# Performance work log

Hardware: AMD Instinct MI355X
Metric: run time of the kernel (lower is better)

## Reference

```python
import jax, jax.numpy as jnp
import numpy as np

B, N, D, H = 8, 1024, 512, 8
DH = D // H  # 64
ALPHA = 0.2  # LeakyReLU slope (args.alpha)
EPS = 1e-6
NEG = -1e9


def layer_norm(x, g, b):
    mean = jnp.mean(x, axis=-1, keepdims=True)
    std = jnp.std(x, axis=-1, keepdims=True)
    return g * (x - mean) / (std + EPS) + b


def setup_inputs() -> dict:
    key = jax.random.key(0)
    ks = jax.random.split(key, 6)
    x = jax.random.normal(ks[0], (B, N, D), dtype=jnp.float32)
    mask = jnp.zeros((B, N), dtype=jnp.int32)  # unused by the block body
    adj = jax.random.randint(ks[1], (B, N, N), 0, 2).astype(jnp.int32)
    W = jax.random.normal(ks[2], (H, D, DH), dtype=jnp.float32) * 0.05
    a_src = jax.random.normal(ks[3], (H, DH), dtype=jnp.float32) * 0.05
    a_dst = jax.random.normal(ks[4], (H, DH), dtype=jnp.float32) * 0.05
    ln1_g = jnp.ones((D,), jnp.float32)
    ln1_b = jnp.zeros((D,), jnp.float32)
    ln2_g = jnp.ones((D,), jnp.float32)
    ln2_b = jnp.zeros((D,), jnp.float32)
    return {"x": x, "mask": mask, "adj": adj, "W": W, "a_src": a_src,
            "a_dst": a_dst, "ln1_g": ln1_g, "ln1_b": ln1_b,
            "ln2_g": ln2_g, "ln2_b": ln2_b}


def ggat(xn, adj, W, a_src, a_dst):
    # multi-head GAT-style attention over dense adjacency (inputP)
    h = jnp.einsum('bnd,hdk->bhnk', xn, W)                 # [B,H,N,DH]
    f_src = jnp.einsum('bhnk,hk->bhn', h, a_src)           # [B,H,N]
    f_dst = jnp.einsum('bhnk,hk->bhn', h, a_dst)
    e = jax.nn.leaky_relu(f_src[..., :, None] + f_dst[..., None, :], ALPHA)
    e = jnp.where(adj[:, None, :, :] > 0, e, NEG)          # mask non-edges
    attn = jax.nn.softmax(e, axis=-1)                      # [B,H,N,N]
    out = jnp.einsum('bhnm,bhmk->bhnk', attn, h)           # aggregate
    out = out.transpose(0, 2, 1, 3).reshape(out.shape[0], out.shape[2], -1)
    return jax.nn.elu(out)                                 # [B,N,D]


def reference(x, mask, adj, W, a_src, a_dst, ln1_g, ln1_b, ln2_g, ln2_b):
    # SublayerConnection: x + dropout(sublayer(norm(x))); dropout = identity (eval)
    xn = layer_norm(x, ln1_g, ln1_b)
    y = x + ggat(xn, adj, W, a_src, a_dst)
    # extra LayerNorm + dropout(identity); module returns (dropout(x), 0)
    y = layer_norm(y, ln2_g, ln2_b)
    return y
```

## Files before the change

### kernel.cpp

```cpp
#include <hip/hip_runtime.h>
#include <stdint.h>

#define B_ 8
#define N_ 1024
#define D_ 512
#define H_ 8
#define DH_ 64


using bf16x8 = __attribute__((ext_vector_type(8))) __bf16;
using f32x4  = __attribute__((ext_vector_type(4))) float;

__device__ __forceinline__ float bf2f(uint32_t u) {
  union { uint32_t u; float f; } c; c.u = u << 16; return c.f;
}
__device__ __forceinline__ uint16_t f2bf(float f) {
  union { float f; uint32_t u; } c; c.f = f;
  return (uint16_t)((c.u + 0x7FFFu + ((c.u >> 16) & 1u)) >> 16);
}
__device__ __forceinline__ void load8f(const void* p, size_t idx, int f32, float v[8]) {
  if (f32) {
    const float4* q = (const float4*)((const float*)p + idx);
    float4 a = q[0], b = q[1];
    v[0]=a.x; v[1]=a.y; v[2]=a.z; v[3]=a.w; v[4]=b.x; v[5]=b.y; v[6]=b.z; v[7]=b.w;
  } else {
    uint4 u = *(const uint4*)((const uint16_t*)p + idx);
    const uint32_t* w = (const uint32_t*)&u;
#pragma unroll
    for (int e = 0; e < 4; e++) { v[2*e] = bf2f(w[e] & 0xffffu); v[2*e+1] = bf2f(w[e] >> 16); }
  }
}
__device__ __forceinline__ float load1f(const void* p, size_t idx, int f32) {
  return f32 ? ((const float*)p)[idx] : bf2f(((const uint16_t*)p)[idx]);
}

__device__ __forceinline__ int detect_f32_block(const uint16_t* x, int t, int* sflag) {
  if (t == 0) *sflag = 0;
  __syncthreads();
  uint2 u = ((const uint2*)x)[t];
  uint32_t bad = 0;
  bad |= (((u.x >> 7)  & 0xffu) >= 0x90u);
  bad |= (((u.x >> 23) & 0xffu) >= 0x90u);
  bad |= (((u.y >> 7)  & 0xffu) >= 0x90u);
  bad |= (((u.y >> 23) & 0xffu) >= 0x90u);
  if (__any(bad)) { if ((t & 63) == 0) atomicOr(sflag, 1); }
  __syncthreads();
  return *sflag;
}

__global__ __launch_bounds__(256) void k_pp(const int* __restrict__ adj,
                                            unsigned long long* __restrict__ adjp,
                                            const uint16_t* __restrict__ xr,
                                            int* __restrict__ flag,
                                            const void* __restrict__ x,
                                            const void* __restrict__ g,
                                            const void* __restrict__ bb,
                                            uint16_t* __restrict__ xn,
                                            const void* __restrict__ W,
                                            uint16_t* __restrict__ Wt) {
  const int bx = blockIdx.x, t = threadIdx.x;
  if (bx < 2048) {
    const int row  = bx * 4 + (t >> 6);
    const int lane = t & 63;
    const int* ar = adj + (size_t)row * N_;
#pragma unroll
    for (int c = 0; c < 16; c++) {
      unsigned long long m = __ballot(ar[c * 64 + lane] > 0);
      if (lane == 0) adjp[(size_t)row * 16 + c] = m;
    }
    return;
  }
  __shared__ int sflag;
  if (bx == 2048) {
    int f32 = detect_f32_block(xr, t, &sflag);
    if (t == 0) *flag = f32;
    return;
  }
  if (bx >= 4097) {
    const int f32 = detect_f32_block(xr, t, &sflag);
    const int bw = bx - 4097;
    const int h = bw >> 3, dt = bw & 7;
    __shared__ uint16_t tile[64][65];
    const size_t sbase = ((size_t)h * D_ + dt * 64) * DH_;
    for (int e = t; e < 4096; e += 256) tile[e >> 6][e & 63] = f2bf(load1f(W, sbase + e, f32));
    __syncthreads();
    uint16_t* dst = Wt + (size_t)h * DH_ * D_ + dt * 64;
    for (int e = t; e < 4096; e += 256) {
      const int k = e >> 6, dd = e & 63;
      dst[(size_t)k * D_ + dd] = tile[dd][k];
    }
    return;
  }
  const int f32 = detect_f32_block(xr, t, &sflag);
  const int row  = (bx - 2049) * 4 + (t >> 6);
  const int lane = t & 63;
  const size_t base = (size_t)row * D_ + lane * 8;
  float v[8]; load8f(x, base, f32, v);
  float s = 0.f, sq = 0.f;
#pragma unroll
  for (int e = 0; e < 8; e++) { s += v[e]; sq += v[e] * v[e]; }
#pragma unroll
  for (int d = 32; d; d >>= 1) { s += __shfl_xor(s, d); sq += __shfl_xor(sq, d); }
  const float mean = s * (1.0f / D_);
  float var = fmaxf(sq * (1.0f / D_) - mean * mean, 0.0f);
  const float inv = 1.0f / (sqrtf(var) + 1e-6f);
  float gv[8], bv[8];
  load8f(g, lane * 8, f32, gv); load8f(bb, lane * 8, f32, bv);
  uint4 ov; uint32_t* ow = (uint32_t*)&ov;
#pragma unroll
  for (int e = 0; e < 4; e++) {
    float o0 = gv[2*e]   * ((v[2*e]   - mean) * inv) + bv[2*e];
    float o1 = gv[2*e+1] * ((v[2*e+1] - mean) * inv) + bv[2*e+1];
    ow[e] = (uint32_t)f2bf(o0) | ((uint32_t)f2bf(o1) << 16);
  }
  *(uint4*)(xn + base) = ov;
}

__global__ __launch_bounds__(256, 2) void k_gemm(const uint16_t* __restrict__ xn,
                                              const uint16_t* __restrict__ Wt,
                                              uint16_t* __restrict__ ht,
                                              const void* __restrict__ asr,
                                              const void* __restrict__ adst,
                                              float* __restrict__ fs,
                                              float* __restrict__ fd,
                                              const int* __restrict__ flag) {
  const int h = blockIdx.x;
  const int r0 = blockIdx.y * 64;
  const int t = threadIdx.x;
  const int wv = t >> 6, lane = t & 63, q = lane >> 4, m16 = lane & 15;
  const int wr = wv >> 1, wc = wv & 1;

  __shared__ union {
    struct { __align__(16) uint16_t A[64 * 72]; __align__(16) uint16_t Bt[64 * 72]; } st;
    __align__(16) uint16_t tr[64 * 72];
  } L;

  f32x4 acc[2][2] = {};
  const int srow = t >> 2, soff = (t & 3) * 16;
  const uint16_t* gA = xn + (size_t)(r0 + srow) * D_ + soff;
  const uint16_t* gB = Wt + ((size_t)h * DH_ + srow) * D_ + soff;
  uint16_t* lA = &L.st.A[srow * 72 + soff];
  uint16_t* lB = &L.st.Bt[srow * 72 + soff];

  for (int k0 = 0; k0 < D_; k0 += 64) {
    uint4 va0 = *(const uint4*)(gA + k0);
    uint4 va1 = *(const uint4*)(gA + k0 + 8);
    uint4 vb0 = *(const uint4*)(gB + k0);
    uint4 vb1 = *(const uint4*)(gB + k0 + 8);
    __syncthreads();
    *(uint4*)lA = va0;  *(uint4*)(lA + 8) = va1;
    *(uint4*)lB = vb0;  *(uint4*)(lB + 8) = vb1;
    __syncthreads();
#pragma unroll
    for (int ks = 0; ks < 2; ks++) {
      bf16x8 a0 = *(const bf16x8*)&L.st.A[(wr * 32 + m16) * 72 + ks * 32 + q * 8];
      bf16x8 a1 = *(const bf16x8*)&L.st.A[(wr * 32 + 16 + m16) * 72 + ks * 32 + q * 8];
      bf16x8 b0 = *(const bf16x8*)&L.st.Bt[(wc * 32 + m16) * 72 + ks * 32 + q * 8];
      bf16x8 b1 = *(const bf16x8*)&L.st.Bt[(wc * 32 + 16 + m16) * 72 + ks * 32 + q * 8];
      acc[0][0] = __builtin_amdgcn_mfma_f32_16x16x32_bf16(a0, b0, acc[0][0], 0, 0, 0);
      acc[0][1] = __builtin_amdgcn_mfma_f32_16x16x32_bf16(a0, b1, acc[0][1], 0, 0, 0);
      acc[1][0] = __builtin_amdgcn_mfma_f32_16x16x32_bf16(a1, b0, acc[1][0], 0, 0, 0);
      acc[1][1] = __builtin_amdgcn_mfma_f32_16x16x32_bf16(a1, b1, acc[1][1], 0, 0, 0);
    }
  }
  __syncthreads();
#pragma unroll
  for (int i2 = 0; i2 < 2; i2++)
#pragma unroll
    for (int j2 = 0; j2 < 2; j2++) {
      f32x4 vv = acc[i2][j2];
      const int sl = wr * 32 + i2 * 16 + q * 4;
      const int kl = wc * 32 + j2 * 16 + m16;
#pragma unroll
      for (int r = 0; r < 4; r++) L.tr[kl * 72 + sl + r] = f2bf(vv[r]);
    }
  __syncthreads();
  const int b = r0 >> 10, n0 = r0 & 1023;
  {
    const int k = t >> 2, ns = (t & 3) * 16;
    const size_t base = (((size_t)b * H_ + h) * DH_ + k) * (size_t)N_ + n0 + ns;
    *(uint4*)(ht + base) = *(const uint4*)&L.tr[k * 72 + ns];
    *(uint4*)(ht + base + 8) = *(const uint4*)&L.tr[k * 72 + ns + 8];
  }
  {
    const int f32 = *flag;
    const int nl = t >> 2, qd = (t & 3) * 16;
    float ss = 0.f, sd = 0.f;
#pragma unroll
    for (int dd = 0; dd < 16; dd++) {
      float hv = bf2f(L.tr[(qd + dd) * 72 + nl]);
      ss = fmaf(hv, load1f(asr,  h * DH_ + qd + dd, f32), ss);
      sd = fmaf(hv, load1f(adst, h * DH_ + qd + dd, f32), sd);
    }
    ss += __shfl_xor(ss, 1); ss += __shfl_xor(ss, 2);
    sd += __shfl_xor(sd, 1); sd += __shfl_xor(sd, 2);
    if ((t & 3) == 0) {
      fs[((size_t)b * H_ + h) * N_ + n0 + nl] = ss;
      fd[((size_t)b * H_ + h) * N_ + n0 + nl] = sd;
    }
  }
}

__global__ __launch_bounds__(256, 2) void k_attn(const uint16_t* __restrict__ ht,
                                                 const float* __restrict__ fs,
                                                 const float* __restrict__ fd,
                                                 const uint32_t* __restrict__ adjp,
                                                 uint16_t* __restrict__ oat) {
  const int bid = blockIdx.x;
  const int bh = bid & 63, itile = bid >> 6;
  const int b = bh >> 3, h = bh & 7;
  const int i0 = itile * 128;
  const int t = threadIdx.x, wv = t >> 6, lane = t & 63, q = lane >> 4, m16 = lane & 15;
  __shared__ __align__(16) uint16_t Hs[64 * 136];
  __shared__ __align__(16) float2 Edi[N_];
  for (int j = t; j < N_; j += 256) {
    float fdv = fd[(size_t)bh * N_ + j];
    Edi[j] = make_float2(exp2f(fdv * 1.44269504f), exp2f(fdv * 0.28853901f));
  }
  const int iA0 = i0 + wv * 32 + m16;
  const int iA1 = iA0 + 16;
  const float fs0 = fs[(size_t)bh * N_ + iA0];
  const float fs1 = fs[(size_t)bh * N_ + iA1];
  const float Es0  = exp2f(fs0 * 1.44269504f), Es20 = exp2f(fs0 * 0.28853901f);
  const float Es1  = exp2f(fs1 * 1.44269504f), Es21 = exp2f(fs1 * 0.28853901f);
  const uint32_t* arow0 = adjp + ((size_t)b * N_ + iA0) * 32;
  const uint32_t* arow1 = adjp + ((size_t)b * N_ + iA1) * 32;
  const uint16_t* gH = ht + (size_t)bh * (DH_ * N_) + (size_t)(t >> 2) * N_ + (t & 3) * 32;
  uint16_t* lH = &Hs[(t >> 2) * 136 + (t & 3) * 32];
  union { uint16_t u[8]; bf16x8 v; } ones;
#pragma unroll
  for (int e = 0; e < 8; e++) ones.u[e] = 0x3F80u;
  f32x4 acc[2][5] = {};
  __syncthreads();
  for (int c = 0; c < 8; c++) {
    const int jc = c * 128;
    uint4 v0 = *(const uint4*)(gH + jc);
    uint4 v1 = *(const uint4*)(gH + jc + 8);
    uint4 v2 = *(const uint4*)(gH + jc + 16);
    uint4 v3 = *(const uint4*)(gH + jc + 24);
    uint4 aw0 = *(const uint4*)(arow0 + c * 4);
    uint4 aw1 = *(const uint4*)(arow1 + c * 4);
    __syncthreads();
    *(uint4*)(lH)      = v0;
    *(uint4*)(lH + 8)  = v1;
    *(uint4*)(lH + 16) = v2;
    *(uint4*)(lH + 24) = v3;
    __syncthreads();
    const uint32_t w0[4] = {aw0.x, aw0.y, aw0.z, aw0.w};
    const uint32_t w1[4] = {aw1.x, aw1.y, aw1.z, aw1.w};
#pragma unroll
    for (int s = 0; s < 4; s++) {
      const int js = s * 32;
      bf16x8 bf0 = *(const bf16x8*)&Hs[(m16)      * 136 + js + q * 8];
      bf16x8 bf1 = *(const bf16x8*)&Hs[(16 + m16) * 136 + js + q * 8];
      bf16x8 bf2 = *(const bf16x8*)&Hs[(32 + m16) * 136 + js + q * 8];
      bf16x8 bf3 = *(const bf16x8*)&Hs[(48 + m16) * 136 + js + q * 8];
      const float2* ed = &Edi[jc + js + q * 8];
      float4 e0 = *(const float4*)(ed);
      float4 e1 = *(const float4*)(ed + 2);
      float4 e2 = *(const float4*)(ed + 4);
      float4 e3 = *(const float4*)(ed + 6);
      const uint32_t ab0 = (w0[s] >> (q * 8)) & 0xffu;
      const uint32_t ab1 = (w1[s] >> (q * 8)) & 0xffu;
#pragma unroll
      for (int f = 0; f < 2; f++) {
        const float Ea  = f ? Es1 : Es0;
        const float Eb  = f ? Es21 : Es20;
        const uint32_t ab = f ? ab1 : ab0;
        float pm[8];
        pm[0] = fmaxf(Ea * e0.x, Eb * e0.y);
        pm[1] = fmaxf(Ea * e0.z, Eb * e0.w);
        pm[2] = fmaxf(Ea * e1.x, Eb * e1.y);
        pm[3] = fmaxf(Ea * e1.z, Eb * e1.w);
        pm[4] = fmaxf(Ea * e2.x, Eb * e2.y);
        pm[5] = fmaxf(Ea * e2.z, Eb * e2.w);
        pm[6] = fmaxf(Ea * e3.x, Eb * e3.y);
        pm[7] = fmaxf(Ea * e3.z, Eb * e3.w);
        union { __bf16 bv[8]; bf16x8 v; } af;
#pragma unroll
        for (int e = 0; e < 8; e++) {
          uint32_t msk = (uint32_t)(((int32_t)(ab << (31 - e))) >> 31);
          af.bv[e] = (__bf16)__uint_as_float(__float_as_uint(pm[e]) & msk);
        }
        acc[f][0] = __builtin_amdgcn_mfma_f32_16x16x32_bf16(af.v, bf0, acc[f][0], 0, 0, 0);
        acc[f][1] = __builtin_amdgcn_mfma_f32_16x16x32_bf16(af.v, bf1, acc[f][1], 0, 0, 0);
        acc[f][2] = __builtin_amdgcn_mfma_f32_16x16x32_bf16(af.v, bf2, acc[f][2], 0, 0, 0);
        acc[f][3] = __builtin_amdgcn_mfma_f32_16x16x32_bf16(af.v, bf3, acc[f][3], 0, 0, 0);
        acc[f][4] = __builtin_amdgcn_mfma_f32_16x16x32_bf16(af.v, ones.v, acc[f][4], 0, 0, 0);
      }
    }
  }
#pragma unroll
  for (int f = 0; f < 2; f++) {
    float linv[4];
#pragma unroll
    for (int r = 0; r < 4; r++) linv[r] = 1.0f / acc[f][4][r];
    const int ibl = i0 + wv * 32 + f * 16 + q * 4;
#pragma unroll
    for (int nt = 0; nt < 4; nt++)
#pragma unroll
      for (int r = 0; r < 4; r++) {
        oat[((size_t)b * N_ + ibl + r) * D_ + h * DH_ + nt * 16 + m16] =
            f2bf(acc[f][nt][r] * linv[r]);
      }
  }
}

__global__ __launch_bounds__(256) void k_final(const void* __restrict__ x,
                                               const uint16_t* __restrict__ oa,
                                               const void* __restrict__ g,
                                               const void* __restrict__ bb,
                                               void* __restrict__ out,
                                               const int* __restrict__ flag) {
  const int f32 = *flag;
  const int row = blockIdx.x * 4 + (threadIdx.x >> 6);
  const int lane = threadIdx.x & 63;
  const size_t base = (size_t)row * D_ + lane * 8;
  float xv[8]; load8f(x, base, f32, xv);
  uint4 av = *(const uint4*)(oa + base);
  const uint32_t* aw = (const uint32_t*)&av;
  float v[8], s = 0.f, sq = 0.f;
#pragma unroll
  for (int e = 0; e < 4; e++) {
    float a0 = bf2f(aw[e] & 0xffffu), a1 = bf2f(aw[e] >> 16);
    a0 = a0 > 0.f ? a0 : exp2f(a0 * 1.44269504f) - 1.0f;
    a1 = a1 > 0.f ? a1 : exp2f(a1 * 1.44269504f) - 1.0f;
    float t0 = xv[2*e] + a0, t1 = xv[2*e+1] + a1;
    v[2*e] = t0; v[2*e+1] = t1;
    s += t0 + t1; sq += t0 * t0 + t1 * t1;
  }
#pragma unroll
  for (int d = 32; d; d >>= 1) { s += __shfl_xor(s, d); sq += __shfl_xor(sq, d); }
  const float mean = s * (1.0f / D_);
  float var = fmaxf(sq * (1.0f / D_) - mean * mean, 0.0f);
  const float inv = 1.0f / (sqrtf(var) + 1e-6f);
  float gv[8], bv[8];
  load8f(g, lane * 8, f32, gv); load8f(bb, lane * 8, f32, bv);
  float r8[8];
#pragma unroll
  for (int e = 0; e < 8; e++) r8[e] = gv[e] * ((v[e] - mean) * inv) + bv[e];
  if (f32) {
    float* o = (float*)out + base;
    float4 o0 = {r8[0], r8[1], r8[2], r8[3]};
    float4 o1 = {r8[4], r8[5], r8[6], r8[7]};
    *(float4*)(o) = o0;
    *(float4*)(o + 4) = o1;
  } else {
    uint4 ov; uint32_t* ow = (uint32_t*)&ov;
#pragma unroll
    for (int e = 0; e < 4; e++)
      ow[e] = (uint32_t)f2bf(r8[2*e]) | ((uint32_t)f2bf(r8[2*e+1]) << 16);
    *(uint4*)((uint16_t*)out + base) = ov;
  }
}

extern "C" void kernel_launch(void* const* d_in, const int* in_sizes, int n_in,
                              void* d_out, int out_size, void* d_ws, size_t ws_size,
                              hipStream_t stream) {
  const void* x = d_in[0];
  const int* adj = (const int*)d_in[2];
  const void* W = d_in[3];
  const void* asr = d_in[4];
  const void* adst = d_in[5];
  const void* g1 = d_in[6];
  const void* b1 = d_in[7];
  const void* g2 = d_in[8];
  const void* b2 = d_in[9];

  uint8_t* ws = (uint8_t*)d_ws;
  uint16_t* ht = (uint16_t*)(ws);
  uint16_t* xn = (uint16_t*)(ws + 8388608);
  uint16_t* oat = xn;
  uint16_t* Wt = (uint16_t*)(ws + 16777216);
  uint32_t* adjp = (uint32_t*)(ws + 17301504);
  float* fs = (float*)(ws + 18350080);
  float* fd = (float*)(ws + 18612224);
  int* flag = (int*)(ws + 18874368);

  k_pp<<<dim3(4161), dim3(256), 0, stream>>>(adj, (unsigned long long*)adjp,
                                             (const uint16_t*)x, flag,
                                             x, g1, b1, xn, W, Wt);
  k_gemm<<<dim3(8, 128), dim3(256), 0, stream>>>(xn, Wt, ht, asr, adst, fs, fd, flag);
  k_attn<<<dim3(512), dim3(256), 0, stream>>>(ht, fs, fd, adjp, oat);
  k_final<<<dim3(2048), dim3(256), 0, stream>>>(x, oat, g2, b2, d_out, flag);
}
```

Measured before the change: 166.7 us.

## Switch intermediates to fp16 with packed-half softmax math and register prefetch

Changes the xn, Wt, ht and attention-output intermediates from bf16 to fp16 and uses f16 MFMA. In the attention kernel the exp-weight products, max and mask are computed with packed half2 ops on fp16 LDS tables instead of per-element fp32 math and bf16 conversion. Both the GEMM and attention loops now prefetch the next tile's global loads into registers before the MMA work on the current tile. fp16 has a narrower range than bf16, so the unnormalised exp products risk overflow or underflow if the scores grow.

```diff
diff --git a/kernel.cpp b/kernel.cpp
--- a/kernel.cpp
+++ b/kernel.cpp
@@ -8,8 +8,9 @@
 #define DH_ 64
 
 
-using bf16x8 = __attribute__((ext_vector_type(8))) __bf16;
-using f32x4  = __attribute__((ext_vector_type(4))) float;
+using f16x8 = __attribute__((ext_vector_type(8))) _Float16;
+using h2    = __attribute__((ext_vector_type(2))) _Float16;
+using f32x4 = __attribute__((ext_vector_type(4))) float;
 
 __device__ __forceinline__ float bf2f(uint32_t u) {
   union { uint32_t u; float f; } c; c.u = u << 16; return c.f;
@@ -17,6 +18,35 @@
 __device__ __forceinline__ uint16_t f2bf(float f) {
   union { float f; uint32_t u; } c; c.f = f;
   return (uint16_t)((c.u + 0x7FFFu + ((c.u >> 16) & 1u)) >> 16);
+}
+__device__ __forceinline__ uint16_t f2h(float f) {
+  union { _Float16 h; uint16_t u; } c; c.h = (_Float16)f; return c.u;
+}
+__device__ __forceinline__ float h2f(uint16_t u) {
+  union { uint16_t u; _Float16 h; } c; c.u = u; return (float)c.h;
+}
+__device__ __forceinline__ uint32_t pk2h(float a, float b) {
+  union { h2 h; uint32_t u; } c; c.h = (h2){(_Float16)a, (_Float16)b}; return c.u;
+}
+__device__ __forceinline__ h2 u2h2(uint32_t u) {
+  union { uint32_t u; h2 h; } c; c.u = u; return c.h;
+}
+__device__ __forceinline__ uint32_t h22u(h2 h) {
+  union { h2 h; uint32_t u; } c; c.h = h; return c.u;
+}
+__device__ __forceinline__ h2 h2splat(float v) {
+  return (h2){(_Float16)v, (_Float16)v};
+}
+__device__ __forceinline__ h2 hmax2(h2 a, h2 b) {
+#if defined(__has_builtin)
+#if __has_builtin(__builtin_elementwise_max)
+  return __builtin_elementwise_max(a, b);
+#else
+  h2 r; r.x = a.x > b.x ? a.x : b.x; r.y = a.y > b.y ? a.y : b.y; return r;
+#endif
+#else
+  h2 r; r.x = a.x > b.x ? a.x : b.x; r.y = a.y > b.y ? a.y : b.y; return r;
+#endif
 }
 __device__ __forceinline__ void load8f(const void* p, size_t idx, int f32, float v[8]) {
   if (f32) {
@@ -82,7 +112,7 @@
     const int h = bw >> 3, dt = bw & 7;
     __shared__ uint16_t tile[64][65];
     const size_t sbase = ((size_t)h * D_ + dt * 64) * DH_;
-    for (int e = t; e < 4096; e += 256) tile[e >> 6][e & 63] = f2bf(load1f(W, sbase + e, f32));
+    for (int e = t; e < 4096; e += 256) tile[e >> 6][e & 63] = f2h(load1f(W, sbase + e, f32));
     __syncthreads();
     uint16_t* dst = Wt + (size_t)h * DH_ * D_ + dt * 64;
     for (int e = t; e < 4096; e += 256) {
@@ -111,7 +141,7 @@
   for (int e = 0; e < 4; e++) {
     float o0 = gv[2*e]   * ((v[2*e]   - mean) * inv) + bv[2*e];
     float o1 = gv[2*e+1] * ((v[2*e+1] - mean) * inv) + bv[2*e+1];
-    ow[e] = (uint32_t)f2bf(o0) | ((uint32_t)f2bf(o1) << 16);
+    ow[e] = (uint32_t)f2h(o0) | ((uint32_t)f2h(o1) << 16);
   }
   *(uint4*)(xn + base) = ov;
 }
@@ -142,25 +172,31 @@
   uint16_t* lA = &L.st.A[srow * 72 + soff];
   uint16_t* lB = &L.st.Bt[srow * 72 + soff];
 
+  uint4 va0 = *(const uint4*)(gA);
+  uint4 va1 = *(const uint4*)(gA + 8);
+  uint4 vb0 = *(const uint4*)(gB);
+  uint4 vb1 = *(const uint4*)(gB + 8);
   for (int k0 = 0; k0 < D_; k0 += 64) {
-    uint4 va0 = *(const uint4*)(gA + k0);
-    uint4 va1 = *(const uint4*)(gA + k0 + 8);
-    uint4 vb0 = *(const uint4*)(gB + k0);
-    uint4 vb1 = *(const uint4*)(gB + k0 + 8);
     __syncthreads();
     *(uint4*)lA = va0;  *(uint4*)(lA + 8) = va1;
     *(uint4*)lB = vb0;  *(uint4*)(lB + 8) = vb1;
     __syncthreads();
+    if (k0 + 64 < D_) {
+      va0 = *(const uint4*)(gA + k0 + 64);
+      va1 = *(const uint4*)(gA + k0 + 72);
+      vb0 = *(const uint4*)(gB + k0 + 64);
+      vb1 = *(const uint4*)(gB + k0 + 72);
+    }
 #pragma unroll
     for (int ks = 0; ks < 2; ks++) {
-      bf16x8 a0 = *(const bf16x8*)&L.st.A[(wr * 32 + m16) * 72 + ks * 32 + q * 8];
-      bf16x8 a1 = *(const bf16x8*)&L.st.A[(wr * 32 + 16 + m16) * 72 + ks * 32 + q * 8];
-      bf16x8 b0 = *(const bf16x8*)&L.st.Bt[(wc * 32 + m16) * 72 + ks * 32 + q * 8];
-      bf16x8 b1 = *(const bf16x8*)&L.st.Bt[(wc * 32 + 16 + m16) * 72 + ks * 32 + q * 8];
-      acc[0][0] = __builtin_amdgcn_mfma_f32_16x16x32_bf16(a0, b0, acc[0][0], 0, 0, 0);
-      acc[0][1] = __builtin_amdgcn_mfma_f32_16x16x32_bf16(a0, b1, acc[0][1], 0, 0, 0);
-      acc[1][0] = __builtin_amdgcn_mfma_f32_16x16x32_bf16(a1, b0, acc[1][0], 0, 0, 0);
-      acc[1][1] = __builtin_amdgcn_mfma_f32_16x16x32_bf16(a1, b1, acc[1][1], 0, 0, 0);
+      f16x8 a0 = *(const f16x8*)&L.st.A[(wr * 32 + m16) * 72 + ks * 32 + q * 8];
+      f16x8 a1 = *(const f16x8*)&L.st.A[(wr * 32 + 16 + m16) * 72 + ks * 32 + q * 8];
+      f16x8 b0 = *(const f16x8*)&L.st.Bt[(wc * 32 + m16) * 72 + ks * 32 + q * 8];
+      f16x8 b1 = *(const f16x8*)&L.st.Bt[(wc * 32 + 16 + m16) * 72 + ks * 32 + q * 8];
+      acc[0][0] = __builtin_amdgcn_mfma_f32_16x16x32_f16(a0, b0, acc[0][0], 0, 0, 0);
+      acc[0][1] = __builtin_amdgcn_mfma_f32_16x16x32_f16(a0, b1, acc[0][1], 0, 0, 0);
+      acc[1][0] = __builtin_amdgcn_mfma_f32_16x16x32_f16(a1, b0, acc[1][0], 0, 0, 0);
+      acc[1][1] = __builtin_amdgcn_mfma_f32_16x16x32_f16(a1, b1, acc[1][1], 0, 0, 0);
     }
   }
   __syncthreads();
@@ -172,7 +208,7 @@
       const int sl = wr * 32 + i2 * 16 + q * 4;
       const int kl = wc * 32 + j2 * 16 + m16;
 #pragma unroll
-      for (int r = 0; r < 4; r++) L.tr[kl * 72 + sl + r] = f2bf(vv[r]);
+      for (int r = 0; r < 4; r++) L.tr[kl * 72 + sl + r] = f2h(vv[r]);
     }
   __syncthreads();
   const int b = r0 >> 10, n0 = r0 & 1023;
@@ -188,7 +224,7 @@
     float ss = 0.f, sd = 0.f;
 #pragma unroll
     for (int dd = 0; dd < 16; dd++) {
-      float hv = bf2f(L.tr[(qd + dd) * 72 + nl]);
+      float hv = h2f(L.tr[(qd + dd) * 72 + nl]);
       ss = fmaf(hv, load1f(asr,  h * DH_ + qd + dd, f32), ss);
       sd = fmaf(hv, load1f(adst, h * DH_ + qd + dd, f32), sd);
     }
@@ -212,81 +248,86 @@
   const int i0 = itile * 128;
   const int t = threadIdx.x, wv = t >> 6, lane = t & 63, q = lane >> 4, m16 = lane & 15;
   __shared__ __align__(16) uint16_t Hs[64 * 136];
-  __shared__ __align__(16) float2 Edi[N_];
-  for (int j = t; j < N_; j += 256) {
-    float fdv = fd[(size_t)bh * N_ + j];
-    Edi[j] = make_float2(exp2f(fdv * 1.44269504f), exp2f(fdv * 0.28853901f));
+  __shared__ __align__(16) uint32_t E1p[N_ / 2];
+  __shared__ __align__(16) uint32_t E2p[N_ / 2];
+  for (int jp = t; jp < N_ / 2; jp += 256) {
+    float2 fv = ((const float2*)(fd + (size_t)bh * N_))[jp];
+    E1p[jp] = pk2h(exp2f(fv.x * 1.44269504f), exp2f(fv.y * 1.44269504f));
+    E2p[jp] = pk2h(exp2f(fv.x * 0.28853901f), exp2f(fv.y * 0.28853901f));
   }
   const int iA0 = i0 + wv * 32 + m16;
   const int iA1 = iA0 + 16;
   const float fs0 = fs[(size_t)bh * N_ + iA0];
   const float fs1 = fs[(size_t)bh * N_ + iA1];
-  const float Es0  = exp2f(fs0 * 1.44269504f), Es20 = exp2f(fs0 * 0.28853901f);
-  const float Es1  = exp2f(fs1 * 1.44269504f), Es21 = exp2f(fs1 * 0.28853901f);
+  const h2 Ea0 = h2splat(exp2f(fs0 * 1.44269504f));
+  const h2 Eb0 = h2splat(exp2f(fs0 * 0.28853901f));
+  const h2 Ea1 = h2splat(exp2f(fs1 * 1.44269504f));
+  const h2 Eb1 = h2splat(exp2f(fs1 * 0.28853901f));
   const uint32_t* arow0 = adjp + ((size_t)b * N_ + iA0) * 32;
   const uint32_t* arow1 = adjp + ((size_t)b * N_ + iA1) * 32;
   const uint16_t* gH = ht + (size_t)bh * (DH_ * N_) + (size_t)(t >> 2) * N_ + (t & 3) * 32;
   uint16_t* lH = &Hs[(t >> 2) * 136 + (t & 3) * 32];
-  union { uint16_t u[8]; bf16x8 v; } ones;
-#pragma unroll
-  for (int e = 0; e < 8; e++) ones.u[e] = 0x3F80u;
+  union { uint16_t u[8]; f16x8 v; } ones;
+#pragma unroll
+  for (int e = 0; e < 8; e++) ones.u[e] = 0x3C00u;
   f32x4 acc[2][5] = {};
-  __syncthreads();
+  uint4 v0 = *(const uint4*)(gH);
+  uint4 v1 = *(const uint4*)(gH + 8);
+  uint4 v2 = *(const uint4*)(gH + 16);
+  uint4 v3 = *(const uint4*)(gH + 24);
+  uint4 aw0 = *(const uint4*)(arow0);
+  uint4 aw1 = *(const uint4*)(arow1);
   for (int c = 0; c < 8; c++) {
-    const int jc = c * 128;
-    uint4 v0 = *(const uint4*)(gH + jc);
-    uint4 v1 = *(const uint4*)(gH + jc + 8);
-    uint4 v2 = *(const uint4*)(gH + jc + 16);
-    uint4 v3 = *(const uint4*)(gH + jc + 24);
-    uint4 aw0 = *(const uint4*)(arow0 + c * 4);
-    uint4 aw1 = *(const uint4*)(arow1 + c * 4);
     __syncthreads();
     *(uint4*)(lH)      = v0;
     *(uint4*)(lH + 8)  = v1;
     *(uint4*)(lH + 16) = v2;
     *(uint4*)(lH + 24) = v3;
     __syncthreads();
-    const uint32_t w0[4] = {aw0.x, aw0.y, aw0.z, aw0.w};
-    const uint32_t w1[4] = {aw1.x, aw1.y, aw1.z, aw1.w};
+    const uint32_t cw0[4] = {aw0.x, aw0.y, aw0.z, aw0.w};
+    const uint32_t cw1[4] = {aw1.x, aw1.y, aw1.z, aw1.w};
+    if (c < 7) {
+      const int jn = (c + 1) * 128;
+      v0 = *(const uint4*)(gH + jn);
+      v1 = *(const uint4*)(gH + jn + 8);
+      v2 = *(const uint4*)(gH + jn + 16);
+      v3 = *(const uint4*)(gH + jn + 24);
+      aw0 = *(const uint4*)(arow0 + (c + 1) * 4);
+      aw1 = *(const uint4*)(arow1 + (c + 1) * 4);
+    }
+    const int eb = c * 64;
 #pragma unroll
     for (int s = 0; s < 4; s++) {
       const int js = s * 32;
-      bf16x8 bf0 = *(const bf16x8*)&Hs[(m16)      * 136 + js + q * 8];
-      bf16x8 bf1 = *(const bf16x8*)&Hs[(16 + m16) * 136 + js + q * 8];
-      bf16x8 bf2 = *(const bf16x8*)&Hs[(32 + m16) * 136 + js + q * 8];
-      bf16x8 bf3 = *(const bf16x8*)&Hs[(48 + m16) * 136 + js + q * 8];
-      const float2* ed = &Edi[jc + js + q * 8];
-      float4 e0 = *(const float4*)(ed);
-      float4 e1 = *(const float4*)(ed + 2);
-      float4 e2 = *(const float4*)(ed + 4);
-      float4 e3 = *(const float4*)(ed + 6);
-      const uint32_t ab0 = (w0[s] >> (q * 8)) & 0xffu;
-      const uint32_t ab1 = (w1[s] >> (q * 8)) & 0xffu;
+      f16x8 hf0 = *(const f16x8*)&Hs[(m16)      * 136 + js + q * 8];
+      f16x8 hf1 = *(const f16x8*)&Hs[(16 + m16) * 136 + js + q * 8];
+      f16x8 hf2 = *(const f16x8*)&Hs[(32 + m16) * 136 + js + q * 8];
+      f16x8 hf3 = *(const f16x8*)&Hs[(48 + m16) * 136 + js + q * 8];
+      const int ei = eb + s * 16 + q * 4;
+      const uint4 e1u = *(const uint4*)&E1p[ei];
+      const uint4 e2u = *(const uint4*)&E2p[ei];
+      const h2 e1[4] = {u2h2(e1u.x), u2h2(e1u.y), u2h2(e1u.z), u2h2(e1u.w)};
+      const h2 e2[4] = {u2h2(e2u.x), u2h2(e2u.y), u2h2(e2u.z), u2h2(e2u.w)};
+      const uint32_t ab0 = (cw0[s] >> (q * 8)) & 0xffu;
+      const uint32_t ab1 = (cw1[s] >> (q * 8)) & 0xffu;
+      const uint32_t t0 = ab0 | (ab0 << 15);
+      const uint32_t t1 = ab1 | (ab1 << 15);
 #pragma unroll
       for (int f = 0; f < 2; f++) {
-        const float Ea  = f ? Es1 : Es0;
-        const float Eb  = f ? Es21 : Es20;
-        const uint32_t ab = f ? ab1 : ab0;
-        float pm[8];
-        pm[0] = fmaxf(Ea * e0.x, Eb * e0.y);
-        pm[1] = fmaxf(Ea * e0.z, Eb * e0.w);
-        pm[2] = fmaxf(Ea * e1.x, Eb * e1.y);
-        pm[3] = fmaxf(Ea * e1.z, Eb * e1.w);
-        pm[4] = fmaxf(Ea * e2.x, Eb * e2.y);
-        pm[5] = fmaxf(Ea * e2.z, Eb * e2.w);
-        pm[6] = fmaxf(Ea * e3.x, Eb * e3.y);
-        pm[7] = fmaxf(Ea * e3.z, Eb * e3.w);
-        union { __bf16 bv[8]; bf16x8 v; } af;
-#pragma unroll
-        for (int e = 0; e < 8; e++) {
-          uint32_t msk = (uint32_t)(((int32_t)(ab << (31 - e))) >> 31);
-          af.bv[e] = (__bf16)__uint_as_float(__float_as_uint(pm[e]) & msk);
+        const h2 Ea = f ? Ea1 : Ea0;
+        const h2 Eb = f ? Eb1 : Eb0;
+        const uint32_t tt = f ? t1 : t0;
+        union { uint32_t u[4]; f16x8 v; } af;
+#pragma unroll
+        for (int p = 0; p < 4; p++) {
+          h2 pm = hmax2(Ea * e1[p], Eb * e2[p]);
+          af.u[p] = h22u(pm) & (((tt >> (2 * p)) & 0x10001u) * 0xFFFFu);
         }
-        acc[f][0] = __builtin_amdgcn_mfma_f32_16x16x32_bf16(af.v, bf0, acc[f][0], 0, 0, 0);
-        acc[f][1] = __builtin_amdgcn_mfma_f32_16x16x32_bf16(af.v, bf1, acc[f][1], 0, 0, 0);
-        acc[f][2] = __builtin_amdgcn_mfma_f32_16x16x32_bf16(af.v, bf2, acc[f][2], 0, 0, 0);
-        acc[f][3] = __builtin_amdgcn_mfma_f32_16x16x32_bf16(af.v, bf3, acc[f][3], 0, 0, 0);
-        acc[f][4] = __builtin_amdgcn_mfma_f32_16x16x32_bf16(af.v, ones.v, acc[f][4], 0, 0, 0);
+        acc[f][0] = __builtin_amdgcn_mfma_f32_16x16x32_f16(af.v, hf0, acc[f][0], 0, 0, 0);
+        acc[f][1] = __builtin_amdgcn_mfma_f32_16x16x32_f16(af.v, hf1, acc[f][1], 0, 0, 0);
+        acc[f][2] = __builtin_amdgcn_mfma_f32_16x16x32_f16(af.v, hf2, acc[f][2], 0, 0, 0);
+        acc[f][3] = __builtin_amdgcn_mfma_f32_16x16x32_f16(af.v, hf3, acc[f][3], 0, 0, 0);
+        acc[f][4] = __builtin_amdgcn_mfma_f32_16x16x32_f16(af.v, ones.v, acc[f][4], 0, 0, 0);
       }
     }
   }
@@ -301,7 +342,7 @@
 #pragma unroll
       for (int r = 0; r < 4; r++) {
         oat[((size_t)b * N_ + ibl + r) * D_ + h * DH_ + nt * 16 + m16] =
-            f2bf(acc[f][nt][r] * linv[r]);
+            f2h(acc[f][nt][r] * linv[r]);
       }
   }
 }
@@ -322,7 +363,8 @@
   float v[8], s = 0.f, sq = 0.f;
 #pragma unroll
   for (int e = 0; e < 4; e++) {
-    float a0 = bf2f(aw[e] & 0xffffu), a1 = bf2f(aw[e] >> 16);
+    float a0 = h2f((uint16_t)(aw[e] & 0xffffu));
+    float a1 = h2f((uint16_t)(aw[e] >> 16));
     a0 = a0 > 0.f ? a0 : exp2f(a0 * 1.44269504f) - 1.0f;
     a1 = a1 > 0.f ? a1 : exp2f(a1 * 1.44269504f) - 1.0f;
     float t0 = xv[2*e] + a0, t1 = xv[2*e+1] + a1;
```

New measurement: 162.0 us. 2.8% less time.
